# Optimization experiments

Hardware: AMD Instinct MI355X
Metric: run time of the kernel (lower is better)

Reference implementation:

```python
import jax, jax.numpy as jnp
import numpy as np

N_Q, N_K, N_HEAD, D_HEAD = 2048, 2048, 8, 64


def setup_inputs() -> dict:
    key = jax.random.key(0)
    kq, kk, ka = jax.random.split(key, 3)
    q = jax.random.normal(kq, (N_Q, N_HEAD, D_HEAD), dtype=jnp.float32)
    k = jax.random.normal(kk, (N_K, N_HEAD, D_HEAD), dtype=jnp.float32)
    # glorot-style init for attn param of shape (1, n_head, 2*d_head)
    fan = N_HEAD * 2 * D_HEAD
    std = float(np.sqrt(6.0 / fan))
    attn = jax.random.uniform(ka, (1, N_HEAD, 2 * D_HEAD), dtype=jnp.float32,
                              minval=-std, maxval=std)
    return {"q": q, "k": k, "attn": attn}


def reference(q, k, attn):
    # attn: (1, n_head, 2*d_head) -> split into query half and key half
    d_head = q.shape[-1]
    a_q = attn[0, :, :d_head]   # (n_head, d_head)
    a_k = attn[0, :, d_head:]   # (n_head, d_head)
    # Additive score without materializing the (n_q, n_k, n_head, 2*d_head)
    # concatenated tensor: score[i,j,h] = relu(q_i_h . a_q_h + k_j_h . a_k_h)
    sq = jnp.einsum("qhd,hd->qh", q, a_q)  # (n_q, n_head)
    sk = jnp.einsum("khd,hd->kh", k, a_k)  # (n_k, n_head)
    scores = jax.nn.relu(sq[:, None, :] + sk[None, :, :])  # (n_q, n_k, n_head)
    # Faithful to original: softmax over dim=-1 at shape (n_q*n_k, n_head),
    # i.e. over the head dimension. mask=None, dropout=0.0.
    return jax.nn.softmax(scores, axis=-1)
```

## Files before the change

### kernel.cpp

```cpp
#include <hip/hip_runtime.h>


#define N_Q   2048
#define N_K   2048
#define N_HEAD 8
#define D_HEAD 64

__global__ __launch_bounds__(256) void proj_kernel(
    const float* __restrict__ q, const float* __restrict__ k,
    const float* __restrict__ attn,
    float* __restrict__ sq, float* __restrict__ sk)
{
    int tid = blockIdx.x * blockDim.x + threadIdx.x;
    int lane8 = tid & 7;
    int pair  = tid >> 3;
    const int PAIRS = N_Q * N_HEAD;
    bool is_k = pair >= PAIRS;
    int p = is_k ? (pair - PAIRS) : pair;
    int h = p & (N_HEAD - 1);

    const float* src = is_k ? k : q;
    const float* a   = attn + h * (2 * D_HEAD) + (is_k ? D_HEAD : 0);

    const float4* s4 = (const float4*)(src + (size_t)p * D_HEAD + lane8 * 8);
    const float4* a4 = (const float4*)(a + lane8 * 8);
    float4 x0 = s4[0], x1 = s4[1];
    float4 w0 = a4[0], w1 = a4[1];
    float sum = x0.x*w0.x + x0.y*w0.y + x0.z*w0.z + x0.w*w0.w
              + x1.x*w1.x + x1.y*w1.y + x1.z*w1.z + x1.w*w1.w;

    sum += __shfl_xor(sum, 1);
    sum += __shfl_xor(sum, 2);
    sum += __shfl_xor(sum, 4);

    if (lane8 == 0) {
        (is_k ? sk : sq)[p] = sum * 1.4426950408889634f;
    }
}

#define SM_BLOCKS 2048
#define SM_ITERS  16

__global__ __launch_bounds__(256) void softmax_kernel(
    const float* __restrict__ sq, const float* __restrict__ sk,
    float* __restrict__ out)
{
    const int STRIDE = SM_BLOCKS * 256;
    int f0 = blockIdx.x * 256 + threadIdx.x;
    int t  = f0 & (2 * N_K - 1);
    int half = f0 & 1;

    float4 kv = ((const float4*)sk)[t];
    const float4* sq4 = (const float4*)sq;
    float4* out4 = (float4*)out;

    #pragma unroll
    for (int it = 0; it < SM_ITERS; ++it) {
        int f = f0 + it * STRIDE;
        int i = f >> 12;
        float4 qv = sq4[2 * i + half];

        float v0 = __builtin_amdgcn_exp2f(fmaxf(qv.x + kv.x, 0.0f));
        float v1 = __builtin_amdgcn_exp2f(fmaxf(qv.y + kv.y, 0.0f));
        float v2 = __builtin_amdgcn_exp2f(fmaxf(qv.z + kv.z, 0.0f));
        float v3 = __builtin_amdgcn_exp2f(fmaxf(qv.w + kv.w, 0.0f));

        float ps = (v0 + v1) + (v2 + v3);
        float s  = ps + __shfl_xor(ps, 1);
        float r  = __builtin_amdgcn_rcpf(s);

        out4[f] = make_float4(v0 * r, v1 * r, v2 * r, v3 * r);
    }
}

extern "C" void kernel_launch(void* const* d_in, const int* in_sizes, int n_in,
                              void* d_out, int out_size, void* d_ws, size_t ws_size,
                              hipStream_t stream) {
    const float* q    = (const float*)d_in[0];
    const float* k    = (const float*)d_in[1];
    const float* attn = (const float*)d_in[2];
    float* out = (float*)d_out;

    float* sq = (float*)d_ws;
    float* sk = sq + N_Q * N_HEAD;

    int total_threads = 2 * N_Q * N_HEAD * 8;
    proj_kernel<<<dim3(total_threads / 256), dim3(256), 0, stream>>>(q, k, attn, sq, sk);

    softmax_kernel<<<dim3(SM_BLOCKS), dim3(256), 0, stream>>>(sq, sk, out);
}
```

Before: 143.1 us.

## Precompute exponentials per row/column and replace per-element exp with multiply-max

Moves the exp2 into the projection kernel, so the softmax kernel computes exp(relu(a+b)) as max(exp(a)*exp(b), 1) and does no per-element transcendental. It also makes the row index wave-uniform through readfirstlane, so the query values come from scalar-friendly loads followed by a select. The xor-1 shuffle is replaced with a DPP quad_perm move. The algebraic identity risks overflow or rounding differences when exp(a)*exp(b) gets large. The kernel is likely store-bandwidth bound, so the gain may be small.

After: 141.9 us. About the same (-0.8%).

```diff
diff --git a/kernel.cpp b/kernel.cpp
--- a/kernel.cpp
+++ b/kernel.cpp
@@ -9,7 +9,7 @@
 __global__ __launch_bounds__(256) void proj_kernel(
     const float* __restrict__ q, const float* __restrict__ k,
     const float* __restrict__ attn,
-    float* __restrict__ sq, float* __restrict__ sk)
+    float* __restrict__ eq, float* __restrict__ ek)
 {
     int tid = blockIdx.x * blockDim.x + threadIdx.x;
     int lane8 = tid & 7;
@@ -34,39 +34,48 @@
     sum += __shfl_xor(sum, 4);
 
     if (lane8 == 0) {
-        (is_k ? sk : sq)[p] = sum * 1.4426950408889634f;
+        float e = __builtin_amdgcn_exp2f(sum * 1.4426950408889634f);
+        (is_k ? ek : eq)[p] = e;
     }
 }
 
 #define SM_BLOCKS 2048
 #define SM_ITERS  16
 
+__device__ __forceinline__ float dpp_xor1(float x) {
+    int v = __builtin_amdgcn_mov_dpp(__builtin_bit_cast(int, x), 0xB1, 0xF, 0xF, true);
+    return __builtin_bit_cast(float, v);
+}
+
 __global__ __launch_bounds__(256) void softmax_kernel(
-    const float* __restrict__ sq, const float* __restrict__ sk,
+    const float* __restrict__ eq, const float* __restrict__ ek,
     float* __restrict__ out)
 {
     const int STRIDE = SM_BLOCKS * 256;
     int f0 = blockIdx.x * 256 + threadIdx.x;
     int t  = f0 & (2 * N_K - 1);
-    int half = f0 & 1;
+    bool h1 = (f0 & 1);
 
-    float4 kv = ((const float4*)sk)[t];
-    const float4* sq4 = (const float4*)sq;
+    float4 kv = ((const float4*)ek)[t];
+    const float4* eq4 = (const float4*)eq;
     float4* out4 = (float4*)out;
 
     #pragma unroll
     for (int it = 0; it < SM_ITERS; ++it) {
         int f = f0 + it * STRIDE;
-        int i = f >> 12;
-        float4 qv = sq4[2 * i + half];
+        int row = __builtin_amdgcn_readfirstlane(f >> 12);
+        float4 e0 = eq4[2 * row];
+        float4 e1 = eq4[2 * row + 1];
+        float4 qv = make_float4(h1 ? e1.x : e0.x, h1 ? e1.y : e0.y,
+                                h1 ? e1.z : e0.z, h1 ? e1.w : e0.w);
 
-        float v0 = __builtin_amdgcn_exp2f(fmaxf(qv.x + kv.x, 0.0f));
-        float v1 = __builtin_amdgcn_exp2f(fmaxf(qv.y + kv.y, 0.0f));
-        float v2 = __builtin_amdgcn_exp2f(fmaxf(qv.z + kv.z, 0.0f));
-        float v3 = __builtin_amdgcn_exp2f(fmaxf(qv.w + kv.w, 0.0f));
+        float v0 = fmaxf(qv.x * kv.x, 1.0f);
+        float v1 = fmaxf(qv.y * kv.y, 1.0f);
+        float v2 = fmaxf(qv.z * kv.z, 1.0f);
+        float v3 = fmaxf(qv.w * kv.w, 1.0f);
 
         float ps = (v0 + v1) + (v2 + v3);
-        float s  = ps + __shfl_xor(ps, 1);
+        float s  = ps + dpp_xor1(ps);
         float r  = __builtin_amdgcn_rcpf(s);
 
         out4[f] = make_float4(v0 * r, v1 * r, v2 * r, v3 * r);
@@ -81,11 +90,11 @@
     const float* attn = (const float*)d_in[2];
     float* out = (float*)d_out;
 
-    float* sq = (float*)d_ws;
-    float* sk = sq + N_Q * N_HEAD;
+    float* eq = (float*)d_ws;
+    float* ek = eq + N_Q * N_HEAD;
 
     int total_threads = 2 * N_Q * N_HEAD * 8;
-    proj_kernel<<<dim3(total_threads / 256), dim3(256), 0, stream>>>(q, k, attn, sq, sk);
+    proj_kernel<<<dim3(total_threads / 256), dim3(256), 0, stream>>>(q, k, attn, eq, ek);
 
-    softmax_kernel<<<dim3(SM_BLOCKS), dim3(256), 0, stream>>>(sq, sk, out);
+    softmax_kernel<<<dim3(SM_BLOCKS), dim3(256), 0, stream>>>(eq, ek, out);
 }
```
